# Performance work log

Hardware: AMD Instinct MI355X
Metric: run time of the kernel (lower is better)

The kernel has to match this reference:

```python
import jax, jax.numpy as jnp
import numpy as np

RADIUS = 1.3
RES = 256
N_INT = 128
STEP = 0.02


def grid_sample3d(grid, coords):
    # grid: [C, D, H, W]; coords: [N, 3] as (x, y, z) in [-1, 1]
    # trilinear, align_corners=True, border clamp (torch grid_sample semantics)
    D, H, W = grid.shape[1], grid.shape[2], grid.shape[3]

    def to_idx(c, size):
        return jnp.clip((c + 1.0) * 0.5 * (size - 1), 0.0, size - 1.0)

    x = to_idx(coords[:, 0], W)
    y = to_idx(coords[:, 1], H)
    z = to_idx(coords[:, 2], D)
    x0 = jnp.floor(x).astype(jnp.int32)
    y0 = jnp.floor(y).astype(jnp.int32)
    z0 = jnp.floor(z).astype(jnp.int32)
    x1 = jnp.minimum(x0 + 1, W - 1)
    y1 = jnp.minimum(y0 + 1, H - 1)
    z1 = jnp.minimum(z0 + 1, D - 1)
    wx = x - x0.astype(x.dtype)
    wy = y - y0.astype(y.dtype)
    wz = z - z0.astype(z.dtype)

    def g(zi, yi, xi):
        return grid[:, zi, yi, xi]  # [C, N]

    c00 = g(z0, y0, x0) * (1 - wx) + g(z0, y0, x1) * wx
    c01 = g(z0, y1, x0) * (1 - wx) + g(z0, y1, x1) * wx
    c10 = g(z1, y0, x0) * (1 - wx) + g(z1, y0, x1) * wx
    c11 = g(z1, y1, x0) * (1 - wx) + g(z1, y1, x1) * wx
    c0 = c00 * (1 - wy) + c01 * wy
    c1 = c10 * (1 - wy) + c11 * wy
    return (c0 * (1 - wz) + c1 * wz).T  # [N, C]


def sh16(d):
    # real spherical harmonics, degree 4 (instant-ngp / tcnn convention), d unit
    x, y, z = d[:, 0], d[:, 1], d[:, 2]
    xx, yy, zz = x * x, y * y, z * z
    xy, yz, xz = x * y, y * z, x * z
    return jnp.stack([
        jnp.full_like(x, 0.28209479177387814),
        -0.48860251190291987 * y,
        0.48860251190291987 * z,
        -0.48860251190291987 * x,
        1.0925484305920792 * xy,
        -1.0925484305920792 * yz,
        0.94617469575755997 * zz - 0.31539156525251999,
        -1.0925484305920792 * xz,
        0.54627421529603959 * (xx - yy),
        0.59004358992664352 * y * (-3.0 * xx + yy),
        2.8906114426405538 * xy * z,
        0.45704579946446572 * y * (1.0 - 5.0 * zz),
        0.3731763325901154 * z * (5.0 * zz - 3.0),
        0.45704579946446572 * x * (1.0 - 5.0 * zz),
        1.445305721320277 * z * (xx - yy),
        0.59004358992664352 * x * (-xx + 3.0 * yy),
    ], axis=-1)  # [N, 16]


def mlp3(x, W0, W1, W2):
    # FullyFusedMLP: no bias, ReLU hidden, linear output
    h = jnp.maximum(x @ W0, 0.0)
    h = jnp.maximum(h @ W1, 0.0)
    return h @ W2


def setup_inputs() -> dict:
    key = jax.random.key(0)
    k = jax.random.split(key, 10)
    B, FD, NF = 4096, 32, 16
    rays_o = jax.random.normal(k[0], (B, 3), jnp.float32) * 0.5
    rays_d = jax.random.normal(k[1], (B, 3), jnp.float32)
    G1 = jax.random.normal(k[2], (3, RES, RES, RES), jnp.float32) * 0.02
    F = jax.random.normal(k[3], (FD, NF, NF, NF), jnp.float32) * 0.05
    W_sig0 = jax.random.normal(k[4], (FD, 128), jnp.float32) / np.sqrt(FD).astype(np.float32)
    W_sig1 = jax.random.normal(k[5], (128, 128), jnp.float32) / np.float32(np.sqrt(128))
    W_sig2 = jax.random.normal(k[6], (128, 16), jnp.float32) / np.float32(np.sqrt(128))
    W_col0 = jax.random.normal(k[7], (31, 64), jnp.float32) / np.float32(np.sqrt(31))
    W_col1 = jax.random.normal(k[8], (64, 64), jnp.float32) / np.float32(np.sqrt(64))
    W_col2 = jax.random.normal(k[9], (64, 3), jnp.float32) / np.float32(np.sqrt(64))
    return {"rays_o": rays_o, "rays_d": rays_d, "G1": G1, "F": F,
            "W_sig0": W_sig0, "W_sig1": W_sig1, "W_sig2": W_sig2,
            "W_col0": W_col0, "W_col1": W_col1, "W_col2": W_col2}


def reference(rays_o, rays_d, G1, F, W_sig0, W_sig1, W_sig2, W_col0, W_col1, W_col2):
    B = rays_o.shape[0]
    d = rays_d / jnp.linalg.norm(rays_d, axis=-1, keepdims=True)
    # ray-sphere intersection |o + t d| = RADIUS (unit d)
    b = jnp.sum(rays_o * d, axis=-1)
    c = jnp.sum(rays_o * rays_o, axis=-1) - RADIUS ** 2
    disc = b * b - c
    hit = disc > 0
    s = jnp.sqrt(jnp.where(hit, disc, 1.0))
    tmin = jnp.where(hit, jnp.maximum(-b - s, 0.0), 0.0)
    tmax = jnp.where(hit, -b + s, 0.0)
    t = tmin[:, None] + jnp.arange(N_INT + 1, dtype=jnp.float32)[None, :] * STEP  # [B, n+1]
    tmid = 0.5 * (t[:, :-1] + t[:, 1:])  # [B, n]
    mask = hit[:, None] & (tmid <= tmax[:, None])  # [B, n]
    pts = rays_o[:, None, :] + d[:, None, :] * tmid[..., None]  # [B, n, 3]
    coords = (pts / RADIUS).reshape(-1, 3)  # in [-1, 1]
    # hash/indirection lookup: G1 gives learned coords into feature grid F
    g1 = grid_sample3d(G1, coords)        # [N, 3]
    feats = grid_sample3d(F, g1)          # [N, 32]
    sig_out = mlp3(feats, W_sig0, W_sig1, W_sig2)  # [N, 16]
    sigma = jnp.where(mask, sig_out[:, 0].reshape(B, N_INT), 0.0)
    sigma = jnp.maximum(sigma, 0.0)
    pd = jnp.broadcast_to(d[:, None, :], (B, N_INT, 3)).reshape(-1, 3)
    enc = sh16(pd)
    col_raw = mlp3(jnp.concatenate([enc, sig_out[:, 1:]], axis=-1), W_col0, W_col1, W_col2)
    col = jnp.where(mask[..., None], col_raw.reshape(B, N_INT, 3), 0.0)
    # volume rendering (sigma2alpha + shrgb2rgb with white background)
    alpha = 1.0 - jnp.exp(-sigma * STEP)
    T = jnp.cumprod(1.0 - alpha + 1e-10, axis=1)
    T_excl = jnp.concatenate([jnp.ones((B, 1), alpha.dtype), T[:, :-1]], axis=1)
    w = alpha * T_excl
    rgb = jnp.einsum('bn,bnc->bc', w, jax.nn.sigmoid(col))
    rgb = rgb + (1.0 - jnp.sum(w, axis=1, keepdims=True))
    return rgb
```

## Files before the change

### kernel.cpp

```cpp
#include <hip/hip_runtime.h>
#include <stdint.h>

#define STEP 0.02f
#define INV_RADIUS (1.0f/1.3f)
#define RADIUS 1.3f

typedef __bf16   bf16x8 __attribute__((ext_vector_type(8)));
typedef float    f32x4  __attribute__((ext_vector_type(4)));
typedef uint32_t u32x4  __attribute__((ext_vector_type(4)));

#define FT_OFF   0
#define W0_OFF   262144
#define W1_OFF   270336
#define W2_OFF   303104
#define C0_OFF   307200
#define C1_OFF   311296
#define C2_OFF   319488

#define FE_BYTES  4096
#define SIG_OFF   8192
#define COL_OFF   8704
#define BLOCK_LDS 10752

__device__ __forceinline__ uint32_t pack2(float a, float b){
    uint32_t ua = __float_as_uint(a); ua += 0x7FFFu + ((ua>>16)&1u);
    uint32_t ub = __float_as_uint(b); ub += 0x7FFFu + ((ub>>16)&1u);
    return (ua>>16) | (ub & 0xFFFF0000u);
}
__device__ __forceinline__ void toidx(float c, float sizem1, int isize,
                                      int& i0, int& i1, float& w){
    float t = (c + 1.f) * 0.5f * sizem1;
    t = fminf(fmaxf(t, 0.f), sizem1);
    float f = floorf(t);
    i0 = (int)f;
    i1 = i0 + 1; if (i1 > isize - 1) i1 = isize - 1;
    w = t - f;
}
__device__ __forceinline__ void lds_fence(){
    asm volatile("s_waitcnt lgkmcnt(0)" ::: "memory");
}
__device__ __forceinline__ uint32_t cvtpk(float lo, float hi){
    uint32_t r;
    asm("v_cvt_pk_bf16_f32 %0, %1, %2" : "=v"(r) : "v"(lo), "v"(hi));
    return r;
}
__device__ __forceinline__ void p32swap(uint32_t& a, uint32_t& b){
    asm("v_permlane32_swap_b32 %0, %1" : "+v"(a), "+v"(b));
}
__device__ __forceinline__ void p16swap(uint32_t& a, uint32_t& b){
    asm("v_permlane16_swap_b32 %0, %1" : "+v"(a), "+v"(b));
}
__device__ __forceinline__ uint32_t pkrelu(float a, float b){
    return cvtpk(fmaxf(a, 0.f), fmaxf(b, 0.f));
}
__device__ __forceinline__ bf16x8 frag_from(uint32_t a, uint32_t b, uint32_t c, uint32_t d){
    union { u32x4 u; bf16x8 h; } cv;
    cv.u = (u32x4){a, b, c, d};
    return cv.h;
}
__device__ __forceinline__ bf16x8 xpose4(const f32x4& t0, const f32x4& t1){
    uint32_t A = pkrelu(t0[0], t0[1]);
    uint32_t B = pkrelu(t0[2], t0[3]);
    uint32_t C = pkrelu(t1[0], t1[1]);
    uint32_t D = pkrelu(t1[2], t1[3]);
    p32swap(A, C); p16swap(A, C);
    p32swap(B, D); p16swap(B, D);
    return frag_from(A, B, C, D);
}

__global__ __launch_bounds__(256) void prep_f(const float* __restrict__ F, uint32_t* __restrict__ ws){
    int idx = blockIdx.x * 256 + threadIdx.x;
    if (idx >= 4096) return;
    uint32_t o[16];
    #pragma unroll
    for (int c = 0; c < 16; c++){
        float a = F[(2*c  )*4096 + idx];
        float b = F[(2*c+1)*4096 + idx];
        o[c] = pack2(a, b);
    }
    uint4* dst = (uint4*)ws;
    #pragma unroll
    for (int q = 0; q < 4; q++)
        dst[idx*4 + q] = make_uint4(o[q*4], o[q*4+1], o[q*4+2], o[q*4+3]);
}

__global__ __launch_bounds__(256) void prep_w(const float* __restrict__ W0, const float* __restrict__ W1,
                                              const float* __restrict__ W2, const float* __restrict__ Wc0,
                                              const float* __restrict__ Wc1, const float* __restrict__ Wc2,
                                              char* __restrict__ ws){
    int gid = blockIdx.x * 256 + threadIdx.x;
    if (gid >= 58*64) return;
    int cg = gid >> 6, lane = gid & 63;
    const float* src; int K, N, base_cg, dstoff;
    if      (cg < 8)  { src = W0;  K = 32;  N = 128; base_cg = 0;  dstoff = W0_OFF; }
    else if (cg < 40) { src = W1;  K = 128; N = 128; base_cg = 8;  dstoff = W1_OFF; }
    else if (cg < 44) { src = W2;  K = 128; N = 16;  base_cg = 40; dstoff = W2_OFF; }
    else if (cg < 48) { src = Wc0; K = 31;  N = 64;  base_cg = 44; dstoff = C0_OFF; }
    else if (cg < 56) { src = Wc1; K = 64;  N = 64;  base_cg = 48; dstoff = C1_OFF; }
    else              { src = Wc2; K = 64;  N = 3;   base_cg = 56; dstoff = C2_OFF; }
    bool c0remap = (cg >= 44 && cg < 48);
    int local = cg - base_cg;
    int NT = (N + 15) >> 4;
    int nt = local % NT, kk = local / NT;
    int n = nt*16 + (lane & 15);
    int kbase = kk*32 + (lane >> 4)*8;
    uint32_t o[4];
    #pragma unroll
    for (int jj = 0; jj < 4; jj++){
        int k0 = kbase + jj*2, k1 = k0 + 1;
        int k0s = (c0remap && k0 > 16) ? k0 - 1 : k0;
        int k1s = (c0remap && k1 > 16) ? k1 - 1 : k1;
        bool v0 = (n < N) && (k0s < K) && !(c0remap && k0 == 16);
        bool v1 = (n < N) && (k1s < K) && !(c0remap && k1 == 16);
        float a = v0 ? src[k0s*N + n] : 0.f;
        float b = v1 ? src[k1s*N + n] : 0.f;
        o[jj] = pack2(a, b);
    }
    uint4* dst = (uint4*)(ws + dstoff);
    dst[local*64 + lane] = make_uint4(o[0], o[1], o[2], o[3]);
}

__global__ __launch_bounds__(128, 4)
void nerf_fused(const float* __restrict__ rays_o, const float* __restrict__ rays_d,
                const float* __restrict__ G1, const char* __restrict__ ws,
                float* __restrict__ out){
    __shared__ __align__(16) char smem[BLOCK_LDS];
    const int tid  = threadIdx.x;
    const int wv   = tid >> 6;
    const int lane = tid & 63;
    const int nl   = lane & 15;
    const int quad = lane >> 4;
    const int ray  = blockIdx.x;
    char*  FEB  = smem + wv*FE_BYTES;
    float* SIGf = (float*)(smem + SIG_OFF);
    float* COLf = (float*)(smem + COL_OFF);

    float ox = rays_o[ray*3+0], oy = rays_o[ray*3+1], oz = rays_o[ray*3+2];
    float rx = rays_d[ray*3+0], ry = rays_d[ray*3+1], rz = rays_d[ray*3+2];
    float nrm = sqrtf(rx*rx + ry*ry + rz*rz);
    float dx = rx/nrm, dy = ry/nrm, dz = rz/nrm;
    float bq = ox*dx + oy*dy + oz*dz;
    float cq = ox*ox + oy*oy + oz*oz - RADIUS*RADIUS;
    float disc = bq*bq - cq;
    bool  hit = disc > 0.f;
    float sq   = sqrtf(hit ? disc : 1.f);
    float tmin = hit ? fmaxf(-bq - sq, 0.f) : 0.f;
    float tmax = hit ? (-bq + sq) : 0.f;

    uint32_t encw0, encw1, encw2, encw3, cinmask;
    {
        float xx=dx*dx, yy=dy*dy, zz=dz*dz, xy=dx*dy, yz=dy*dz, xz=dx*dz;
        float sh0 = 0.28209479177387814f;
        float sh1 = -0.48860251190291987f*dy;
        float sh2 =  0.48860251190291987f*dz;
        float sh3 = -0.48860251190291987f*dx;
        float sh4 =  1.0925484305920792f*xy;
        float sh5 = -1.0925484305920792f*yz;
        float sh6 =  0.94617469575756f*zz - 0.31539156525252f;
        float sh7 = -1.0925484305920792f*xz;
        float sh8 =  0.5462742152960396f*(xx-yy);
        float sh9 =  0.5900435899266435f*dy*(-3.f*xx+yy);
        float sh10 = 2.890611442640554f*xy*dz;
        float sh11 = 0.4570457994644657f*dy*(1.f-5.f*zz);
        float sh12 = 0.3731763325901154f*dz*(5.f*zz-3.f);
        float sh13 = 0.4570457994644657f*dx*(1.f-5.f*zz);
        float sh14 = 1.445305721320277f*dz*(xx-yy);
        float sh15 = 0.5900435899266435f*dx*(-xx+3.f*yy);
        bool q0 = (quad == 0);
        encw0 = q0 ? pack2(sh0, sh1) : pack2(sh8,  sh9);
        encw1 = q0 ? pack2(sh2, sh3) : pack2(sh10, sh11);
        encw2 = q0 ? pack2(sh4, sh5) : pack2(sh12, sh13);
        encw3 = q0 ? pack2(sh6, sh7) : pack2(sh14, sh15);
        cinmask = (quad == 2) ? 0xFFFF0000u : 0xFFFFFFFFu;
    }

    const char* pW0 = ws + W0_OFF; const char* pW1 = ws + W1_OFF; const char* pW2 = ws + W2_OFF;
    const char* pC0 = ws + C0_OFF; const char* pC1 = ws + C1_OFF; const char* pC2 = ws + C2_OFF;
    const f32x4 vzero = {0.f, 0.f, 0.f, 0.f};

    #define RD_A(bp, linRow, m) \
        (*(const bf16x8*)((bp) + (linRow)*64 + ((quad ^ (((m)>>1)&3))*16)))
    #define LD_B(base, kk, NT, nt) \
        (*(const bf16x8*)((base) + (((kk)*(NT) + (nt))*64 + lane)*16))

    float Dn = (tmax - tmin) * (1.0f/STEP);
    int nv = (int)fminf(128.f, fmaxf(0.f, floorf(Dn + 0.5f) + 1.f));
    int rem = nv - wv*64;
    if (rem > 64) rem = 64;

    if (rem > 0){
        {
            if (lane < rem){
                int p = wv*64 + lane;
                float tmid = tmin + ((float)p + 0.5f) * STEP;
                float px = (ox + dx*tmid) * INV_RADIUS;
                float py = (oy + dy*tmid) * INV_RADIUS;
                float pz = (oz + dz*tmid) * INV_RADIUS;
                int x0,x1,y0,y1,z0,z1; float wx,wy,wz;
                toidx(px, 255.f, 256, x0, x1, wx);
                toidx(py, 255.f, 256, y0, y1, wy);
                toidx(pz, 255.f, 256, z0, z1, wz);
                float g1v[3];
                #pragma unroll
                for (int ch = 0; ch < 3; ch++){
                    const float* gp = G1 + ch*16777216;
                    int b00 = (z0*256 + y0)*256, b01 = (z0*256 + y1)*256;
                    int b10 = (z1*256 + y0)*256, b11 = (z1*256 + y1)*256;
                    float c000 = gp[b00+x0], c001 = gp[b00+x1];
                    float c010 = gp[b01+x0], c011 = gp[b01+x1];
                    float c100 = gp[b10+x0], c101 = gp[b10+x1];
                    float c110 = gp[b11+x0], c111 = gp[b11+x1];
                    float c00 = c000 + (c001-c000)*wx;
                    float c01 = c010 + (c011-c010)*wx;
                    float c10 = c100 + (c101-c100)*wx;
                    float c11 = c110 + (c111-c110)*wx;
                    float c0 = c00 + (c01-c00)*wy;
                    float c1 = c10 + (c11-c10)*wy;
                    g1v[ch] = c0 + (c1-c0)*wz;
                }
                int fx0,fx1,fy0,fy1,fz0,fz1; float fwx,fwy,fwz;
                toidx(g1v[0], 15.f, 16, fx0, fx1, fwx);
                toidx(g1v[1], 15.f, 16, fy0, fy1, fwy);
                toidx(g1v[2], 15.f, 16, fz0, fz1, fwz);
                float feats[32];
                #pragma unroll
                for (int i = 0; i < 32; i++) feats[i] = 0.f;
                const uint4* Ft = (const uint4*)(ws + FT_OFF);
                #pragma unroll 2
                for (int corner = 0; corner < 8; corner++){
                    int cz = (corner>>2)&1, cy = (corner>>1)&1, cx = corner&1;
                    int xi = cx?fx1:fx0, yi = cy?fy1:fy0, zi = cz?fz1:fz0;
                    float w = (cx?fwx:1.f-fwx) * (cy?fwy:1.f-fwy) * (cz?fwz:1.f-fwz);
                    const uint4* cp = Ft + ((zi*16 + yi)*16 + xi)*4;
                    #pragma unroll
                    for (int q = 0; q < 4; q++){
                        uint4 v = cp[q];
                        uint32_t u[4] = {v.x, v.y, v.z, v.w};
                        #pragma unroll
                        for (int e = 0; e < 4; e++){
                            feats[q*8 + e*2    ] += w * __uint_as_float(u[e] << 16);
                            feats[q*8 + e*2 + 1] += w * __uint_as_float(u[e] & 0xFFFF0000u);
                        }
                    }
                }
                int fsw = (lane>>1)&3;
                #pragma unroll
                for (int c = 0; c < 4; c++){
                    uint4 v = make_uint4(pack2(feats[c*8+0], feats[c*8+1]),
                                         pack2(feats[c*8+2], feats[c*8+3]),
                                         pack2(feats[c*8+4], feats[c*8+5]),
                                         pack2(feats[c*8+6], feats[c*8+7]));
                    *(uint4*)(FEB + lane*64 + ((c^fsw)*16)) = v;
                }
            }
        }
        lds_fence();

        bf16x8 bW2[4], bC0[4], bC2[2];
        #pragma unroll
        for (int kk = 0; kk < 4; kk++) bW2[kk] = LD_B(pW2, kk, 1, 0);
        #pragma unroll
        for (int nt = 0; nt < 4; nt++) bC0[nt] = LD_B(pC0, 0, 4, nt);
        #pragma unroll
        for (int kk = 0; kk < 2; kk++) bC2[kk] = LD_B(pC2, kk, 1, 0);

        int mtmax = (rem + 15) >> 4;
        #pragma unroll 1
        for (int mt = 0; mt < mtmax; mt++){
            const int mArow = mt*16 + nl;
            const int tb = wv*64 + mt*16;

            bf16x8 fe = RD_A(FEB, mArow, mArow);
            f32x4 a0[8];
            #pragma unroll
            for (int nt = 0; nt < 8; nt++)
                a0[nt] = __builtin_amdgcn_mfma_f32_16x16x32_bf16(LD_B(pW0,0,8,nt), fe, vzero, 0,0,0);
            bf16x8 h1[4];
            #pragma unroll
            for (int kk = 0; kk < 4; kk++)
                h1[kk] = xpose4(a0[2*kk], a0[2*kk+1]);

            f32x4 a1[8];
            #pragma unroll
            for (int nt = 0; nt < 8; nt++) a1[nt] = vzero;
            #pragma unroll
            for (int kk = 0; kk < 4; kk++)
                #pragma unroll
                for (int nt = 0; nt < 8; nt++)
                    a1[nt] = __builtin_amdgcn_mfma_f32_16x16x32_bf16(LD_B(pW1,kk,8,nt), h1[kk], a1[nt], 0,0,0);
            bf16x8 h2[4];
            #pragma unroll
            for (int kk = 0; kk < 4; kk++)
                h2[kk] = xpose4(a1[2*kk], a1[2*kk+1]);

            f32x4 sacc = vzero;
            #pragma unroll
            for (int kk = 0; kk < 4; kk++)
                sacc = __builtin_amdgcn_mfma_f32_16x16x32_bf16(bW2[kk], h2[kk], sacc, 0,0,0);
            if (quad == 0) SIGf[tb + nl] = sacc[0];

            uint32_t ca = cvtpk(sacc[0], sacc[1]);
            uint32_t cb = cvtpk(sacc[2], sacc[3]);
            p32swap(ca, cb); p16swap(ca, cb);
            uint32_t cw0 = encw0, cw2 = encw2;
            p32swap(cw0, ca);
            p32swap(cw2, cb);
            cw0 &= cinmask;
            uint32_t cw1 = (quad < 2) ? encw1 : ca;
            uint32_t cw3 = (quad < 2) ? encw3 : cb;
            bf16x8 cin = frag_from(cw0, cw1, cw2, cw3);

            f32x4 c0[4];
            #pragma unroll
            for (int nt = 0; nt < 4; nt++)
                c0[nt] = __builtin_amdgcn_mfma_f32_16x16x32_bf16(bC0[nt], cin, vzero, 0,0,0);
            bf16x8 g1[2];
            #pragma unroll
            for (int kk = 0; kk < 2; kk++)
                g1[kk] = xpose4(c0[2*kk], c0[2*kk+1]);

            f32x4 c1[4];
            #pragma unroll
            for (int nt = 0; nt < 4; nt++) c1[nt] = vzero;
            #pragma unroll
            for (int kk = 0; kk < 2; kk++)
                #pragma unroll
                for (int nt = 0; nt < 4; nt++)
                    c1[nt] = __builtin_amdgcn_mfma_f32_16x16x32_bf16(LD_B(pC1,kk,4,nt), g1[kk], c1[nt], 0,0,0);
            bf16x8 g2[2];
            #pragma unroll
            for (int kk = 0; kk < 2; kk++)
                g2[kk] = xpose4(c1[2*kk], c1[2*kk+1]);

            f32x4 cc = vzero;
            #pragma unroll
            for (int kk = 0; kk < 2; kk++)
                cc = __builtin_amdgcn_mfma_f32_16x16x32_bf16(bC2[kk], g2[kk], cc, 0,0,0);
            if (quad == 0){
                *(float2*)(COLf + (tb + nl)*4) = make_float2(cc[0], cc[1]);
                COLf[(tb + nl)*4 + 2] = cc[2];
            }
        }
    }

    __syncthreads();

    if (wv != 0) return;

    float t0 = tmin + ((float)lane + 0.5f) * STEP;
    float t1 = tmin + ((float)(lane + 64) + 0.5f) * STEP;
    bool  m0 = hit && (t0 <= tmax);
    bool  m1 = hit && (t1 <= tmax);
    float sig0 = m0 ? fmaxf(SIGf[lane], 0.f) : 0.f;
    float sig1 = m1 ? fmaxf(SIGf[lane + 64], 0.f) : 0.f;
    float e0 = expf(-sig0 * STEP), e1 = expf(-sig1 * STEP);
    float al0 = 1.f - e0, al1 = 1.f - e1;
    float li0 = logf(e0 + 1e-10f), li1 = logf(e1 + 1e-10f);
    float incl0 = li0, incl1 = li1;
    #pragma unroll
    for (int off = 1; off < 64; off <<= 1){
        float v0 = __shfl_up(incl0, off);
        float v1 = __shfl_up(incl1, off);
        if (lane >= off){ incl0 += v0; incl1 += v1; }
    }
    float tot0 = __shfl(incl0, 63);
    float ex0 = incl0 - li0;
    float ex1 = tot0 + incl1 - li1;
    float w0 = al0 * expf(ex0);
    float w1 = al1 * expf(ex1);
    float cr0 = m0 ? COLf[lane*4+0] : 0.f;
    float cg0 = m0 ? COLf[lane*4+1] : 0.f;
    float cb0 = m0 ? COLf[lane*4+2] : 0.f;
    float cr1 = m1 ? COLf[(lane+64)*4+0] : 0.f;
    float cg1 = m1 ? COLf[(lane+64)*4+1] : 0.f;
    float cb1 = m1 ? COLf[(lane+64)*4+2] : 0.f;
    float r = w0 / (1.f + expf(-cr0)) + w1 / (1.f + expf(-cr1));
    float g = w0 / (1.f + expf(-cg0)) + w1 / (1.f + expf(-cg1));
    float b = w0 / (1.f + expf(-cb0)) + w1 / (1.f + expf(-cb1));
    float wa = w0 + w1;
    #pragma unroll
    for (int off = 32; off > 0; off >>= 1){
        r  += __shfl_xor(r,  off);
        g  += __shfl_xor(g,  off);
        b  += __shfl_xor(b,  off);
        wa += __shfl_xor(wa, off);
    }
    if (lane == 0){
        out[ray*3+0] = r + (1.f - wa);
        out[ray*3+1] = g + (1.f - wa);
        out[ray*3+2] = b + (1.f - wa);
    }
    #undef RD_A
    #undef LD_B
}

extern "C" void kernel_launch(void* const* d_in, const int* in_sizes, int n_in,
                              void* d_out, int out_size, void* d_ws, size_t ws_size,
                              hipStream_t stream){
    const float* rays_o = (const float*)d_in[0];
    const float* rays_d = (const float*)d_in[1];
    const float* G1     = (const float*)d_in[2];
    const float* F      = (const float*)d_in[3];
    prep_f<<<16, 256, 0, stream>>>(F, (uint32_t*)d_ws);
    prep_w<<<15, 256, 0, stream>>>((const float*)d_in[4], (const float*)d_in[5],
                                   (const float*)d_in[6], (const float*)d_in[7],
                                   (const float*)d_in[8], (const float*)d_in[9],
                                   (char*)d_ws);
    nerf_fused<<<4096, 128, 0, stream>>>(rays_o, rays_d, G1, (const char*)d_ws, (float*)d_out);
}
```

Before: 428.5 us.

## Repack G1 into interleaved bf16 channel layout for vectorized trilinear fetches

Adds a prep kernel that converts the three-channel fp32 G1 grid into an interleaved bf16 layout with two adjacent x voxels per 16-byte load. The main kernel then fetches each of the four x-row pairs with a single vector load instead of 24 scattered scalar loads. The intent is to cut the number of gather transactions in the main kernel. In exchange, every call reads the full 192MB G1 and writes 128MB, which may cost more than it saves. G1 is also rounded to bf16, and the occupancy hint in launch bounds drops from 4 to 2.

```diff
diff --git a/kernel.cpp b/kernel.cpp
--- a/kernel.cpp
+++ b/kernel.cpp
@@ -8,6 +8,7 @@
 typedef __bf16   bf16x8 __attribute__((ext_vector_type(8)));
 typedef float    f32x4  __attribute__((ext_vector_type(4)));
 typedef uint32_t u32x4  __attribute__((ext_vector_type(4)));
+typedef uint32_t u32x4a __attribute__((ext_vector_type(4), aligned(8)));
 
 #define FT_OFF   0
 #define W0_OFF   262144
@@ -16,6 +17,8 @@
 #define C0_OFF   307200
 #define C1_OFF   311296
 #define C2_OFF   319488
+#define G1T_OFF  321536
+#define WS_NEED  (321536ull + 134217728ull)
 
 #define FE_BYTES  4096
 #define SIG_OFF   8192
@@ -27,6 +30,8 @@
     uint32_t ub = __float_as_uint(b); ub += 0x7FFFu + ((ub>>16)&1u);
     return (ua>>16) | (ub & 0xFFFF0000u);
 }
+__device__ __forceinline__ float bfl(uint32_t u){ return __uint_as_float(u << 16); }
+__device__ __forceinline__ float bfh(uint32_t u){ return __uint_as_float(u & 0xFFFF0000u); }
 __device__ __forceinline__ void toidx(float c, float sizem1, int isize,
                                       int& i0, int& i1, float& w){
     float t = (c + 1.f) * 0.5f * sizem1;
@@ -66,6 +71,26 @@
     p32swap(A, C); p16swap(A, C);
     p32swap(B, D); p16swap(B, D);
     return frag_from(A, B, C, D);
+}
+__device__ __forceinline__ void rowlerp(const u32x4a d, bool xe, float wx,
+                                        float& v0, float& v1, float& v2){
+    uint32_t a01 = xe ? d[2] : d[0];
+    uint32_t a2w = xe ? d[3] : d[1];
+    float a0 = bfl(a01), a1 = bfh(a01), a2 = bfl(a2w);
+    float b0 = bfl(d[2]), b1 = bfh(d[2]), b2 = bfl(d[3]);
+    v0 = a0 + (b0 - a0)*wx;
+    v1 = a1 + (b1 - a1)*wx;
+    v2 = a2 + (b2 - a2)*wx;
+}
+
+__global__ __launch_bounds__(256) void prep_g1(const float* __restrict__ G1, uint32_t* __restrict__ dst){
+    int idx2 = (blockIdx.x*256 + threadIdx.x)*2;
+    float2 a = *(const float2*)(G1 + idx2);
+    float2 b = *(const float2*)(G1 + idx2 + 16777216);
+    float2 c = *(const float2*)(G1 + idx2 + 33554432);
+    uint4 o = make_uint4(pack2(a.x, b.x), pack2(c.x, 0.f),
+                         pack2(a.y, b.y), pack2(c.y, 0.f));
+    *(uint4*)(dst + idx2*2) = o;
 }
 
 __global__ __launch_bounds__(256) void prep_f(const float* __restrict__ F, uint32_t* __restrict__ ws){
@@ -120,7 +145,8 @@
     dst[local*64 + lane] = make_uint4(o[0], o[1], o[2], o[3]);
 }
 
-__global__ __launch_bounds__(128, 4)
+template<bool G1PACK>
+__global__ __launch_bounds__(128, 2)
 void nerf_fused(const float* __restrict__ rays_o, const float* __restrict__ rays_d,
                 const float* __restrict__ G1, const char* __restrict__ ws,
                 float* __restrict__ out){
@@ -201,22 +227,45 @@
                 toidx(py, 255.f, 256, y0, y1, wy);
                 toidx(pz, 255.f, 256, z0, z1, wz);
                 float g1v[3];
-                #pragma unroll
-                for (int ch = 0; ch < 3; ch++){
-                    const float* gp = G1 + ch*16777216;
-                    int b00 = (z0*256 + y0)*256, b01 = (z0*256 + y1)*256;
-                    int b10 = (z1*256 + y0)*256, b11 = (z1*256 + y1)*256;
-                    float c000 = gp[b00+x0], c001 = gp[b00+x1];
-                    float c010 = gp[b01+x0], c011 = gp[b01+x1];
-                    float c100 = gp[b10+x0], c101 = gp[b10+x1];
-                    float c110 = gp[b11+x0], c111 = gp[b11+x1];
-                    float c00 = c000 + (c001-c000)*wx;
-                    float c01 = c010 + (c011-c010)*wx;
-                    float c10 = c100 + (c101-c100)*wx;
-                    float c11 = c110 + (c111-c110)*wx;
-                    float c0 = c00 + (c01-c00)*wy;
-                    float c1 = c10 + (c11-c10)*wy;
-                    g1v[ch] = c0 + (c1-c0)*wz;
+                if constexpr (G1PACK){
+                    const uint32_t* Gt = (const uint32_t*)(ws + G1T_OFF);
+                    int xs = (x0 < 255) ? x0 : 254;
+                    bool xe = (x0 == 255);
+                    int r00 = (z0*256 + y0)*256 + xs, r01 = (z0*256 + y1)*256 + xs;
+                    int r10 = (z1*256 + y0)*256 + xs, r11 = (z1*256 + y1)*256 + xs;
+                    u32x4a d00 = *(const u32x4a*)(Gt + (size_t)r00*2);
+                    u32x4a d01 = *(const u32x4a*)(Gt + (size_t)r01*2);
+                    u32x4a d10 = *(const u32x4a*)(Gt + (size_t)r10*2);
+                    u32x4a d11 = *(const u32x4a*)(Gt + (size_t)r11*2);
+                    float v00x,v00y,v00z, v01x,v01y,v01z, v10x,v10y,v10z, v11x,v11y,v11z;
+                    rowlerp(d00, xe, wx, v00x, v00y, v00z);
+                    rowlerp(d01, xe, wx, v01x, v01y, v01z);
+                    rowlerp(d10, xe, wx, v10x, v10y, v10z);
+                    rowlerp(d11, xe, wx, v11x, v11y, v11z);
+                    float c0x = v00x + (v01x - v00x)*wy, c1x = v10x + (v11x - v10x)*wy;
+                    float c0y = v00y + (v01y - v00y)*wy, c1y = v10y + (v11y - v10y)*wy;
+                    float c0z = v00z + (v01z - v00z)*wy, c1z = v10z + (v11z - v10z)*wy;
+                    g1v[0] = c0x + (c1x - c0x)*wz;
+                    g1v[1] = c0y + (c1y - c0y)*wz;
+                    g1v[2] = c0z + (c1z - c0z)*wz;
+                } else {
+                    #pragma unroll
+                    for (int ch = 0; ch < 3; ch++){
+                        const float* gp = G1 + ch*16777216;
+                        int b00 = (z0*256 + y0)*256, b01 = (z0*256 + y1)*256;
+                        int b10 = (z1*256 + y0)*256, b11 = (z1*256 + y1)*256;
+                        float c000 = gp[b00+x0], c001 = gp[b00+x1];
+                        float c010 = gp[b01+x0], c011 = gp[b01+x1];
+                        float c100 = gp[b10+x0], c101 = gp[b10+x1];
+                        float c110 = gp[b11+x0], c111 = gp[b11+x1];
+                        float c00 = c000 + (c001-c000)*wx;
+                        float c01 = c010 + (c011-c010)*wx;
+                        float c10 = c100 + (c101-c100)*wx;
+                        float c11 = c110 + (c111-c110)*wx;
+                        float c0 = c00 + (c01-c00)*wy;
+                        float c1 = c10 + (c11-c10)*wy;
+                        g1v[ch] = c0 + (c1-c0)*wz;
+                    }
                 }
                 int fx0,fx1,fy0,fy1,fz0,fz1; float fwx,fwy,fwz;
                 toidx(g1v[0], 15.f, 16, fx0, fx1, fwx);
@@ -401,10 +450,16 @@
     const float* rays_d = (const float*)d_in[1];
     const float* G1     = (const float*)d_in[2];
     const float* F      = (const float*)d_in[3];
+    bool fast = (ws_size >= WS_NEED);
+    if (fast)
+        prep_g1<<<32768, 256, 0, stream>>>(G1, (uint32_t*)((char*)d_ws + G1T_OFF));
     prep_f<<<16, 256, 0, stream>>>(F, (uint32_t*)d_ws);
     prep_w<<<15, 256, 0, stream>>>((const float*)d_in[4], (const float*)d_in[5],
                                    (const float*)d_in[6], (const float*)d_in[7],
                                    (const float*)d_in[8], (const float*)d_in[9],
                                    (char*)d_ws);
-    nerf_fused<<<4096, 128, 0, stream>>>(rays_o, rays_d, G1, (const char*)d_ws, (float*)d_out);
-}
+    if (fast)
+        nerf_fused<true><<<4096, 128, 0, stream>>>(rays_o, rays_d, G1, (const char*)d_ws, (float*)d_out);
+    else
+        nerf_fused<false><<<4096, 128, 0, stream>>>(rays_o, rays_d, G1, (const char*)d_ws, (float*)d_out);
+}
```

Measured after the change: 384.0 us. 1.12x faster.
